# Performance work log

Measured on AMD Instinct MI355X. Metric: run time of the kernel, lower is better.

## Reference

```python
import jax, jax.numpy as jnp
import numpy as np


def setup_inputs() -> dict:
    key = jax.random.key(0)
    k1, k2, k3 = jax.random.split(key, 3)
    N, F, C, E = 100000, 256, 64, 3200000
    x = jax.random.normal(k1, (N, F), dtype=jnp.float32)
    edge_index = jax.random.randint(k2, (2, E), 0, N, dtype=jnp.int64)
    W = jax.random.normal(k3, (F, C), dtype=jnp.float32) * (1.0 / np.sqrt(F))
    b = jnp.zeros((C,), dtype=jnp.float32)
    return {"x": x, "edge_index": edge_index, "W": W, "b": b}


def reference(x, edge_index, W, b):
    N = x.shape[0]
    # Linear transform first (GCNConv: x @ W)
    xw = x @ W  # [N, C]
    # gcn_norm: add self-loops with weight 1
    loops = jnp.arange(N, dtype=edge_index.dtype)
    src = jnp.concatenate([edge_index[0], loops])
    dst = jnp.concatenate([edge_index[1], loops])
    ones = jnp.ones(src.shape[0], dtype=xw.dtype)
    deg = jax.ops.segment_sum(ones, dst, num_segments=N)  # in-degree incl. self-loop
    deg_inv_sqrt = jnp.where(deg > 0, jax.lax.rsqrt(deg), 0.0)
    norm = deg_inv_sqrt[src] * deg_inv_sqrt[dst]  # [E+N]
    # Message: norm * x_j, then MEAN aggregation over destinations (aggr='mean')
    msg = xw[src] * norm[:, None]  # [E+N, C]
    agg = jax.ops.segment_sum(msg, dst, num_segments=N)  # [N, C]
    cnt = jnp.maximum(deg, 1.0)  # number of incoming messages per node
    out = agg / cnt[:, None] + b
    return jax.nn.log_softmax(out, axis=1)
```

## Files before the change

kernel.cpp:

```cpp
#include <hip/hip_runtime.h>


#define C_DIM 64
#define F_DIM 256
#define TILE 128
#define BIN_PT 16
#define BIN_TILE_E 4096
#define SORT_CAP 6144
#define SMEM_BYTES 36880

#if __has_builtin(__builtin_amdgcn_cvt_pk_f32_fp8) && __has_builtin(__builtin_amdgcn_cvt_pk_fp8_f32)
#define USE_FP8 1
#endif

typedef __attribute__((ext_vector_type(8))) short bf16x8;
typedef __attribute__((ext_vector_type(2))) short bf16x2;
typedef __attribute__((ext_vector_type(4))) float f32x4;
typedef __attribute__((ext_vector_type(2))) float f32x2;

static __device__ __forceinline__ unsigned short f2bf(float f) {
    unsigned int u = __float_as_uint(f);
    unsigned int r = (u + 0x7FFFu + ((u >> 16) & 1u)) >> 16;
    return (unsigned short)r;
}
static __device__ __forceinline__ float u2lo(unsigned int u) {
    return __uint_as_float(u << 16);
}
static __device__ __forceinline__ float u2hi(unsigned int u) {
    return __uint_as_float(u & 0xFFFF0000u);
}

#if !defined(USE_FP8)
#if __has_builtin(__builtin_amdgcn_fdot2_f32_bf16)
static __device__ __forceinline__ void acc_pair(unsigned int u, float& lo, float& hi) {
    union { unsigned int ui; bf16x2 v; } p;
    p.ui = u;
    const bf16x2 SEL_LO = { (short)0x3F80, (short)0 };
    const bf16x2 SEL_HI = { (short)0, (short)0x3F80 };
    lo = __builtin_amdgcn_fdot2_f32_bf16(p.v, SEL_LO, lo, false);
    hi = __builtin_amdgcn_fdot2_f32_bf16(p.v, SEL_HI, hi, false);
}
#else
static __device__ __forceinline__ void acc_pair(unsigned int u, float& lo, float& hi) {
    lo += u2lo(u);
    hi += u2hi(u);
}
#endif
#endif


__global__ void k_zero1(int* __restrict__ a, int N) {
    int i = blockIdx.x * blockDim.x + threadIdx.x;
    if (i < N) a[i] = 0;
}

__global__ void k_zero2(int* __restrict__ a, int* __restrict__ b, int N) {
    int i = blockIdx.x * blockDim.x + threadIdx.x;
    if (i < N) { a[i] = 0; b[i] = 0; }
}

__global__ void k_count(const int* __restrict__ ei, int* __restrict__ degE, int E) {
    int stride = gridDim.x * blockDim.x;
    for (int e = blockIdx.x * blockDim.x + threadIdx.x; e < E; e += stride)
        atomicAdd(&degE[ei[E + e]], 1);
}

__global__ void k_dis2(const int* __restrict__ degE, float* __restrict__ dis, int N) {
    int i = blockIdx.x * blockDim.x + threadIdx.x;
    if (i < N) dis[i] = rsqrtf((float)(degE[i] + 1));
}


__global__ void k_prep(const float* __restrict__ W, unsigned short* __restrict__ Wt,
                       int* __restrict__ gcur, int K) {
    int i = blockIdx.x * blockDim.x + threadIdx.x;
    int c = i & 63, k = i >> 6;
    Wt[(size_t)c * F_DIM + k] = f2bf(W[(size_t)k * C_DIM + c]);
    if (i < K) gcur[i] = i * SORT_CAP;
}


__launch_bounds__(256)
__global__ void k_bin_gemm(const int* __restrict__ ei, int* __restrict__ gcur,
                           unsigned int* __restrict__ colb,
                           const float* __restrict__ x,
                           const unsigned short* __restrict__ Wt,
                           void* __restrict__ yout,
                           int E, int K, int nTiles, int gemmBlocks, int N) {
    __shared__ __align__(16) char smem[SMEM_BYTES];
    const int t = threadIdx.x;

    if (blockIdx.x < gemmBlocks) {
        float4 (*xs2)[1024] = (float4 (*)[1024])smem;
        const int wv   = t >> 6;
        const int lane = t & 63;
        const int lr   = lane & 15;
        const int lq   = lane >> 4;
        const int row0 = blockIdx.x * 64;

        auto stagefn = [&](int buf, int kk) {
            #pragma unroll
            for (int j = 0; j < 4; ++j) {
                int base_idx = j * 256 + wv * 64;
                int idx = base_idx + lane;
                int r   = idx >> 4;
                int c4  = idx & 15;
                int sc4 = c4 ^ (r & 15);
                int gr  = row0 + r;
                if (gr >= N) gr = N - 1;
                const float* g = x + (size_t)gr * F_DIM + kk * 64 + sc4 * 4;
                float4* lbase = &xs2[buf][base_idx];
                __builtin_amdgcn_global_load_lds(
                    (const __attribute__((address_space(1))) unsigned int*)g,
                    (__attribute__((address_space(3))) unsigned int*)lbase,
                    16, 0, 0);
            }
        };

        f32x4 acc[4] = {};

        stagefn(0, 0);
        __syncthreads();

        for (int kk = 0; kk < 4; ++kk) {
            if (kk < 3) stagefn((kk + 1) & 1, kk + 1);

            const float4* rowp = &xs2[kk & 1][(wv * 16 + lr) * 16];
            #pragma unroll
            for (int kc2 = 0; kc2 < 2; ++kc2) {
                int c4 = kc2 * 8 + lq * 2;
                float4 f0 = rowp[c4 ^ lr];
                float4 f1 = rowp[(c4 + 1) ^ lr];
                union { bf16x8 v; unsigned int u[4]; } a;
                a.u[0] = (unsigned)f2bf(f0.x) | ((unsigned)f2bf(f0.y) << 16);
                a.u[1] = (unsigned)f2bf(f0.z) | ((unsigned)f2bf(f0.w) << 16);
                a.u[2] = (unsigned)f2bf(f1.x) | ((unsigned)f2bf(f1.y) << 16);
                a.u[3] = (unsigned)f2bf(f1.z) | ((unsigned)f2bf(f1.w) << 16);
                const int kglob = kk * 64 + kc2 * 32 + lq * 8;
                #pragma unroll
                for (int cb = 0; cb < 4; ++cb) {
                    bf16x8 bfr = *(const bf16x8*)(Wt + (size_t)(cb * 16 + lr) * F_DIM + kglob);
                    acc[cb] = __builtin_amdgcn_mfma_f32_16x16x32_bf16(a.v, bfr, acc[cb], 0, 0, 0);
                }
            }
            __syncthreads();
        }

        const int rbase = row0 + wv * 16 + lq * 4;
        #pragma unroll
        for (int j = 0; j < 4; ++j) {
            int r = rbase + j;
            if (r < N) {
#ifdef USE_FP8
                unsigned char* yf = (unsigned char*)yout;
                #pragma unroll
                for (int cb = 0; cb < 4; ++cb) {
                    float v = acc[cb][j];
                    int p = __builtin_amdgcn_cvt_pk_fp8_f32(v, v, 0, false);
                    yf[(size_t)r * C_DIM + cb * 16 + lr] = (unsigned char)(p & 0xFF);
                }
#else
                unsigned short* ybp = (unsigned short*)yout;
                #pragma unroll
                for (int cb = 0; cb < 4; ++cb)
                    ybp[(size_t)r * C_DIM + cb * 16 + lr] = f2bf(acc[cb][j]);
#endif
            }
        }
        return;
    }

    {
        int* hcnt  = (int*)smem;
        int* hoff  = (int*)(smem + 4096);
        int* gbase = (int*)(smem + 8192);
        int* wps   = (int*)(smem + 12288);
        unsigned int*  stage    = (unsigned int*)(smem + 12304);
        unsigned short* stage_bk = (unsigned short*)(smem + 28688);
        const int wv = t >> 6;
        const int ln = t & 63;

        const int e0 = (blockIdx.x - gemmBlocks) * BIN_TILE_E;
        const int nE = min(BIN_TILE_E, E - e0);
        hcnt[t] = 0; hcnt[t + 256] = 0; hcnt[t + 512] = 0; hcnt[t + 768] = 0;
        __syncthreads();

        unsigned int pk[BIN_PT];
        int bk[BIN_PT];
        int off[BIN_PT];
        #pragma unroll
        for (int j = 0; j < BIN_PT; ++j) {
            int e = e0 + j * 256 + t;
            if (e < E) {
                int s = ei[e];
                int d = ei[E + e];
                int k = d >> 7;
                bk[j]  = k;
                pk[j]  = ((unsigned)(d & 127) << 25) | (unsigned)s;
                off[j] = atomicAdd(&hcnt[k], 1);
            } else bk[j] = -1;
        }
        __syncthreads();

        int a0 = hcnt[t*4], a1 = hcnt[t*4+1], a2 = hcnt[t*4+2], a3 = hcnt[t*4+3];
        int s4 = a0 + a1 + a2 + a3;
        int incl = s4;
        #pragma unroll
        for (int o = 1; o < 64; o <<= 1) {
            int u = __shfl_up(incl, o, 64);
            if (ln >= o) incl += u;
        }
        if (ln == 63) wps[wv] = incl;
        __syncthreads();
        int wpre = 0;
        #pragma unroll
        for (int w = 0; w < 4; ++w)
            if (w < wv) wpre += wps[w];
        int eb = wpre + incl - s4;
        hoff[t*4+0] = eb;
        hoff[t*4+1] = eb + a0;
        hoff[t*4+2] = eb + a0 + a1;
        hoff[t*4+3] = eb + a0 + a1 + a2;
        __syncthreads();

        #pragma unroll
        for (int j = 0; j < BIN_PT; ++j)
            if (bk[j] >= 0) {
                int p = hoff[bk[j]] + off[j];
                stage[p] = pk[j];
                stage_bk[p] = (unsigned short)bk[j];
            }

        for (int kq = t; kq < K; kq += 256) {
            int c = hcnt[kq];
            gbase[kq] = (c > 0) ? atomicAdd(&gcur[kq], c) : 0;
        }
        __syncthreads();

        for (int i = t; i < nE; i += 256) {
            int bb = stage_bk[i];
            int idx = gbase[bb] + (i - hoff[bb]);
            if (idx < (bb + 1) * SORT_CAP)
                colb[idx] = stage[i];
        }
    }
}


__launch_bounds__(256)
__global__ void k_sort(unsigned int* __restrict__ colb,
                       const int* __restrict__ gcur,
                       int* __restrict__ rowptr, int* __restrict__ rowcnt,
                       float* __restrict__ dis,
                       unsigned int* __restrict__ yw,
                       int N, int K) {
    __shared__ unsigned int scache[SORT_CAP];
    __shared__ int ncnt[TILE];
    __shared__ int nscan[TILE];
    __shared__ int ncur[TILE];
    __shared__ float sdis[TILE];
    const int t = threadIdx.x;
    const int k = blockIdx.x;
    const int base = k * SORT_CAP;
    const int cnt  = min(gcur[k] - base, SORT_CAP);
    const int node0 = k << 7;

    if (t < TILE) ncnt[t] = 0;
    __syncthreads();
    for (int i = t; i < cnt; i += 256) {
        unsigned int pk = colb[base + i];
        scache[i] = pk;
        atomicAdd(&ncnt[pk >> 25], 1);
    }
    __syncthreads();

    if (t < TILE) nscan[t] = ncnt[t];
    __syncthreads();
    for (int o = 1; o < TILE; o <<= 1) {
        int v = 0;
        if (t < TILE && t >= o) v = nscan[t - o];
        __syncthreads();
        if (t < TILE) nscan[t] += v;
        __syncthreads();
    }
    if (t < TILE) {
        int ex = nscan[t] - ncnt[t];
        ncur[t] = ex;
        int node = node0 + t;
        if (node < N) {
            rowptr[node] = base + ex;
            rowcnt[node] = ncnt[t];
            float d = rsqrtf((float)(ncnt[t] + 1));
            dis[node] = d;
            sdis[t] = d;
        }
    }
    __syncthreads();

    for (int i = t; i < cnt; i += 256) {
        unsigned int pk = scache[i];
        int dl  = (int)(pk >> 25);
        int pos = atomicAdd(&ncur[dl], 1);
        colb[base + pos] = pk & 0x1FFFFFFu;
    }

    const int nrows = min(TILE, N - node0);
#ifdef USE_FP8
    unsigned int* yrow = yw + (size_t)node0 * 16;
    for (int u = t; u < nrows * 16; u += 256) {
        int r = u >> 4;
        float d = sdis[r];
        unsigned int v = yrow[u];
        f32x2 lo = __builtin_amdgcn_cvt_pk_f32_fp8((int)v, false);
        f32x2 hi = __builtin_amdgcn_cvt_pk_f32_fp8((int)v, true);
        int p = __builtin_amdgcn_cvt_pk_fp8_f32(lo.x * d, lo.y * d, 0, false);
        p = __builtin_amdgcn_cvt_pk_fp8_f32(hi.x * d, hi.y * d, p, true);
        yrow[u] = (unsigned int)p;
    }
#else
    unsigned int* yrow = yw + (size_t)node0 * 32;
    for (int u = t; u < nrows * 32; u += 256) {
        int r = u >> 5;
        unsigned int v = yrow[u];
        float d = sdis[r];
        unsigned short lo = f2bf(u2lo(v) * d);
        unsigned short hi = f2bf(u2hi(v) * d);
        yrow[u] = ((unsigned int)hi << 16) | lo;
    }
#endif
}


__launch_bounds__(256)
__global__ void k_agg(const int* __restrict__ rowptr, const int* __restrict__ rowcnt,
                      const int* __restrict__ col,
                      const void* __restrict__ yin, const float* __restrict__ dis,
                      const float* __restrict__ b, float* __restrict__ out, int N) {
    const int lane = threadIdx.x & 63;
    const int g    = lane >> 3;
    const int cl   = lane & 7;
    int row = blockIdx.x * 4 + (threadIdx.x >> 6);
    if (row >= N) return;
    const int start = rowptr[row];
    const int cntE  = rowcnt[row];
    const int end   = start + cntE;

    float a0, a1, a2, a3, a4, a5, a6, a7;

#ifdef USE_FP8
    const uint2* yv = (const uint2*)yin;
    f32x2 p01 = {0.f, 0.f}, p23 = {0.f, 0.f}, p45 = {0.f, 0.f}, p67 = {0.f, 0.f};
    if (g == 0) {
        uint2 u = yv[(size_t)row * 8 + cl];
        p01 = __builtin_amdgcn_cvt_pk_f32_fp8((int)u.x, false);
        p23 = __builtin_amdgcn_cvt_pk_f32_fp8((int)u.x, true);
        p45 = __builtin_amdgcn_cvt_pk_f32_fp8((int)u.y, false);
        p67 = __builtin_amdgcn_cvt_pk_f32_fp8((int)u.y, true);
    }
    int i = start + g;
    for (; i + 24 < end; i += 32) {
        int s[4];
        #pragma unroll
        for (int j = 0; j < 4; ++j) s[j] = col[i + 8 * j];
        uint2 v[4];
        #pragma unroll
        for (int j = 0; j < 4; ++j) v[j] = yv[(size_t)s[j] * 8 + cl];
        #pragma unroll
        for (int j = 0; j < 4; ++j) {
            p01 += __builtin_amdgcn_cvt_pk_f32_fp8((int)v[j].x, false);
            p23 += __builtin_amdgcn_cvt_pk_f32_fp8((int)v[j].x, true);
            p45 += __builtin_amdgcn_cvt_pk_f32_fp8((int)v[j].y, false);
            p67 += __builtin_amdgcn_cvt_pk_f32_fp8((int)v[j].y, true);
        }
    }
    for (; i < end; i += 8) {
        uint2 u = yv[(size_t)col[i] * 8 + cl];
        p01 += __builtin_amdgcn_cvt_pk_f32_fp8((int)u.x, false);
        p23 += __builtin_amdgcn_cvt_pk_f32_fp8((int)u.x, true);
        p45 += __builtin_amdgcn_cvt_pk_f32_fp8((int)u.y, false);
        p67 += __builtin_amdgcn_cvt_pk_f32_fp8((int)u.y, true);
    }
    a0 = p01.x; a1 = p01.y; a2 = p23.x; a3 = p23.y;
    a4 = p45.x; a5 = p45.y; a6 = p67.x; a7 = p67.y;
#else
    const uint4* yv = (const uint4*)yin;
    a0 = a1 = a2 = a3 = a4 = a5 = a6 = a7 = 0.f;
    if (g == 0) {
        uint4 u = yv[(size_t)row * 8 + cl];
        a0 = u2lo(u.x); a1 = u2hi(u.x); a2 = u2lo(u.y); a3 = u2hi(u.y);
        a4 = u2lo(u.z); a5 = u2hi(u.z); a6 = u2lo(u.w); a7 = u2hi(u.w);
    }
    int i = start + g;
    for (; i + 24 < end; i += 32) {
        int s[4];
        #pragma unroll
        for (int j = 0; j < 4; ++j) s[j] = col[i + 8 * j];
        uint4 v[4];
        #pragma unroll
        for (int j = 0; j < 4; ++j) v[j] = yv[(size_t)s[j] * 8 + cl];
        #pragma unroll
        for (int j = 0; j < 4; ++j) {
            acc_pair(v[j].x, a0, a1);
            acc_pair(v[j].y, a2, a3);
            acc_pair(v[j].z, a4, a5);
            acc_pair(v[j].w, a6, a7);
        }
    }
    for (; i < end; i += 8) {
        uint4 u = yv[(size_t)col[i] * 8 + cl];
        acc_pair(u.x, a0, a1);
        acc_pair(u.y, a2, a3);
        acc_pair(u.z, a4, a5);
        acc_pair(u.w, a6, a7);
    }
#endif

    #pragma unroll
    for (int o = 8; o <= 32; o <<= 1) {
        a0 += __shfl_xor(a0, o, 64); a1 += __shfl_xor(a1, o, 64);
        a2 += __shfl_xor(a2, o, 64); a3 += __shfl_xor(a3, o, 64);
        a4 += __shfl_xor(a4, o, 64); a5 += __shfl_xor(a5, o, 64);
        a6 += __shfl_xor(a6, o, 64); a7 += __shfl_xor(a7, o, 64);
    }

    const float scale = dis[row] / (float)(cntE + 1);
    const float4 b0 = *(const float4*)&b[8 * cl];
    const float4 b1 = *(const float4*)&b[8 * cl + 4];
    float v0 = a0 * scale + b0.x;
    float v1 = a1 * scale + b0.y;
    float v2 = a2 * scale + b0.z;
    float v3 = a3 * scale + b0.w;
    float v4 = a4 * scale + b1.x;
    float v5 = a5 * scale + b1.y;
    float v6 = a6 * scale + b1.z;
    float v7 = a7 * scale + b1.w;

    float m = fmaxf(fmaxf(fmaxf(v0, v1), fmaxf(v2, v3)),
                    fmaxf(fmaxf(v4, v5), fmaxf(v6, v7)));
    #pragma unroll
    for (int o = 4; o >= 1; o >>= 1) m = fmaxf(m, __shfl_xor(m, o, 64));
    float ss = __expf(v0 - m) + __expf(v1 - m) + __expf(v2 - m) + __expf(v3 - m)
             + __expf(v4 - m) + __expf(v5 - m) + __expf(v6 - m) + __expf(v7 - m);
    #pragma unroll
    for (int o = 4; o >= 1; o >>= 1) ss += __shfl_xor(ss, o, 64);
    float lg = logf(ss);

    if (g == 0) {
        float* orow = out + (size_t)row * C_DIM + 8 * cl;
        *(float4*)(orow + 0) = make_float4(v0 - m - lg, v1 - m - lg, v2 - m - lg, v3 - m - lg);
        *(float4*)(orow + 4) = make_float4(v4 - m - lg, v5 - m - lg, v6 - m - lg, v7 - m - lg);
    }
}


__launch_bounds__(256, 4)
__global__ void k_gemmF(const float* __restrict__ x, const float* __restrict__ W,
                        const float* __restrict__ dis, float* __restrict__ y, int N) {
    __shared__ float xs[64 * 68];
    __shared__ float ws[64 * 64];
    const int t   = threadIdx.x;
    const int c16 = t & 15;
    const int rg  = t >> 4;
    const int row0 = blockIdx.x * 64;

    float acc[4][4] = {};

    for (int kk = 0; kk < F_DIM / 64; ++kk) {
        {
            int r  = t >> 2;
            int fq = (t & 3) * 16;
            int grow = row0 + r;
            float4 v0, v1, v2, v3;
            if (grow < N) {
                const float* src = x + (long long)grow * F_DIM + kk * 64 + fq;
                v0 = *(const float4*)(src + 0);
                v1 = *(const float4*)(src + 4);
                v2 = *(const float4*)(src + 8);
                v3 = *(const float4*)(src + 12);
            } else {
                v0 = v1 = v2 = v3 = make_float4(0.f, 0.f, 0.f, 0.f);
            }
            float4* dstp = (float4*)&xs[r * 68 + fq];
            dstp[0] = v0; dstp[1] = v1; dstp[2] = v2; dstp[3] = v3;
        }
        {
            int f  = t >> 2;
            int cq = (t & 3) * 16;
            const float* src = W + (long long)(kk * 64 + f) * C_DIM + cq;
            float4* dstp = (float4*)&ws[f * 64 + cq];
            dstp[0] = *(const float4*)(src + 0);
            dstp[1] = *(const float4*)(src + 4);
            dstp[2] = *(const float4*)(src + 8);
            dstp[3] = *(const float4*)(src + 12);
        }
        __syncthreads();

        const float4* xs4 = (const float4*)xs;
        const float4* ws4 = (const float4*)ws;
        #pragma unroll
        for (int f4 = 0; f4 < 16; ++f4) {
            float xr[4][4];
            #pragma unroll
            for (int k = 0; k < 4; ++k) {
                float4 v = xs4[(rg * 4 + k) * 17 + f4];
                xr[k][0] = v.x; xr[k][1] = v.y; xr[k][2] = v.z; xr[k][3] = v.w;
            }
            #pragma unroll
            for (int j = 0; j < 4; ++j) {
                float4 wv = ws4[(f4 * 4 + j) * 16 + c16];
                #pragma unroll
                for (int k = 0; k < 4; ++k) {
                    acc[k][0] += xr[k][j] * wv.x;
                    acc[k][1] += xr[k][j] * wv.y;
                    acc[k][2] += xr[k][j] * wv.z;
                    acc[k][3] += xr[k][j] * wv.w;
                }
            }
        }
        __syncthreads();
    }

    const int c = c16 * 4;
    #pragma unroll
    for (int k = 0; k < 4; ++k) {
        int row = row0 + rg * 4 + k;
        if (row < N) {
            float dd = dis[row];
            float4 v = make_float4(acc[k][0]*dd, acc[k][1]*dd, acc[k][2]*dd, acc[k][3]*dd);
            *(float4*)&y[(size_t)row * C_DIM + c] = v;
        }
    }
}

__global__ void k_scan_blk(const int* __restrict__ degE, int* __restrict__ excl,
                           int* __restrict__ bsum, int N) {
    __shared__ int sm[1024];
    const int tid = threadIdx.x;
    int i = blockIdx.x * 1024 + tid;
    int v = (i < N) ? degE[i] : 0;
    sm[tid] = v;
    __syncthreads();
    for (int off = 1; off < 1024; off <<= 1) {
        int t = (tid >= off) ? sm[tid - off] : 0;
        __syncthreads();
        sm[tid] += t;
        __syncthreads();
    }
    int incl = sm[tid];
    if (i < N) excl[i] = incl - v;
    if (tid == 1023) bsum[blockIdx.x] = incl;
}

__global__ void k_scan_top(int* __restrict__ bs, int nblk) {
    __shared__ int sm[128];
    const int tid = threadIdx.x;
    int v = (tid < nblk) ? bs[tid] : 0;
    sm[tid] = v;
    __syncthreads();
    for (int off = 1; off < 128; off <<= 1) {
        int t = (tid >= off) ? sm[tid - off] : 0;
        __syncthreads();
        sm[tid] += t;
        __syncthreads();
    }
    if (tid < nblk) bs[tid] = sm[tid] - v;
}

__global__ void k_scan_add(const int* __restrict__ excl, const int* __restrict__ bs,
                           int* __restrict__ rowptr, int N, int E) {
    int i = blockIdx.x * blockDim.x + threadIdx.x;
    if (i < N) rowptr[i] = excl[i] + bs[i >> 10];
    if (i == 0) rowptr[N] = E;
}

__global__ void k_scatter(const int* __restrict__ ei, const int* __restrict__ rowptr,
                          int* __restrict__ cnt, int* __restrict__ col, int E) {
    int stride = gridDim.x * blockDim.x;
    for (int e = blockIdx.x * blockDim.x + threadIdx.x; e < E; e += stride) {
        int s = ei[e];
        int d = ei[E + e];
        int p = atomicAdd(&cnt[d], 1);
        col[rowptr[d] + p] = s;
    }
}

__global__ void k_aggB(const int* __restrict__ rowptr, const int* __restrict__ col,
                       const float* __restrict__ y, const float* __restrict__ dis,
                       const float* __restrict__ b, float* __restrict__ out, int N) {
    const int lane = threadIdx.x & 63;
    int row = blockIdx.x * 4 + (threadIdx.x >> 6);
    if (row >= N) return;
    const int start = rowptr[row], end = rowptr[row + 1];
    float acc = y[(size_t)row * C_DIM + lane];
    for (int i = start; i < end; ++i) acc += y[(size_t)col[i] * C_DIM + lane];
    float val = acc * dis[row] / (float)(end - start + 1) + b[lane];
    float m = val;
    #pragma unroll
    for (int o = 32; o >= 1; o >>= 1) m = fmaxf(m, __shfl_xor(m, o, 64));
    float ex = expf(val - m);
    float ss = ex;
    #pragma unroll
    for (int o = 32; o >= 1; o >>= 1) ss += __shfl_xor(ss, o, 64);
    out[(size_t)row * C_DIM + lane] = val - m - logf(ss);
}

__global__ void k_selfloop2(const float* __restrict__ y, const float* __restrict__ dis,
                            float* __restrict__ agg, int NC) {
    int i = blockIdx.x * blockDim.x + threadIdx.x;
    if (i < NC) agg[i] = dis[i >> 6] * y[i];
}

__launch_bounds__(256)
__global__ void k_edge2(const int* __restrict__ ei, const float* __restrict__ y,
                        const float* __restrict__ dis, float* __restrict__ agg, int E) {
    const int lane = threadIdx.x & 63;
    int wid = (blockIdx.x * blockDim.x + threadIdx.x) >> 6;
    int nw  = (gridDim.x * blockDim.x) >> 6;
    for (int e = wid; e < E; e += nw) {
        int s = ei[e];
        int d = ei[E + e];
        atomicAdd(&agg[(size_t)d * C_DIM + lane], y[(size_t)s * C_DIM + lane] * dis[d]);
    }
}

__launch_bounds__(256)
__global__ void k_final2(float* __restrict__ agg, const int* __restrict__ degE,
                         const float* __restrict__ b, int N) {
    const int lane = threadIdx.x & 63;
    int row = blockIdx.x * 4 + (threadIdx.x >> 6);
    if (row >= N) return;
    float v = agg[(size_t)row * C_DIM + lane] / (float)(degE[row] + 1) + b[lane];
    float m = v;
    #pragma unroll
    for (int o = 32; o >= 1; o >>= 1) m = fmaxf(m, __shfl_xor(m, o, 64));
    float ex = expf(v - m);
    float ss = ex;
    #pragma unroll
    for (int o = 32; o >= 1; o >>= 1) ss += __shfl_xor(ss, o, 64);
    agg[(size_t)row * C_DIM + lane] = v - m - logf(ss);
}


extern "C" void kernel_launch(void* const* d_in, const int* in_sizes, int n_in,
                              void* d_out, int out_size, void* d_ws, size_t ws_size,
                              hipStream_t stream) {
    const float* x  = (const float*)d_in[0];
    const int*   ei = (const int*)d_in[1];
    const float* W  = (const float*)d_in[2];
    const float* b  = (const float*)d_in[3];

    const int C = in_sizes[3];
    const int F = in_sizes[2] / C;
    const int N = in_sizes[0] / F;
    const int E = in_sizes[1] / 2;

    float* out = (float*)d_out;
    char*  wsb = (char*)d_ws;

    const int K    = (N + TILE - 1) / TILE;
    const int nblk = (N + 1023) / 1024;

    size_t offA = 0;
    void*  yv   = (void*)(wsb + offA);    offA += ((size_t)N * C * 2 + 15) & ~15ull;
    unsigned short* Wt = (unsigned short*)(wsb + offA); offA += ((size_t)F * C * 2 + 15) & ~15ull;
    float* disA   = (float*)(wsb + offA); offA += (size_t)N * 4;
    int*   rowptrA= (int*)(wsb + offA);   offA += (size_t)N * 4;
    int*   rowcntA= (int*)(wsb + offA);   offA += (size_t)N * 4;
    int*   gcur   = (int*)(wsb + offA);   offA += (size_t)K * 4;
    unsigned int* colb = (unsigned int*)(wsb + offA); offA += (size_t)K * SORT_CAP * 4;

    size_t offB = 0;
    float* yB     = (float*)(wsb + offB); offB += (size_t)N * C * 4;
    float* disB   = (float*)(wsb + offB); offB += (size_t)N * 4;
    int*   rowptrB= (int*)(wsb + offB);   offB += ((size_t)N + 1) * 4;
    int*   degE   = (int*)(wsb + offB);   offB += (size_t)N * 4;
    int*   cntB   = (int*)(wsb + offB);   offB += (size_t)N * 4;
    int*   excl   = (int*)(wsb + offB);   offB += (size_t)nblk * 1024 * 4;
    int*   bsum   = (int*)(wsb + offB);   offB += 128 * 4;
    int*   colB   = (int*)(wsb + offB);   offB += (size_t)E * 4;

    const bool okA = (offA <= ws_size) && (K <= 1024) && (N < (1 << 25)) &&
                     (C == 64) && (F == 256) &&
                     ((long long)E < (long long)K * SORT_CAP);
    const bool okB = (offB <= ws_size) && (nblk <= 128);

    const dim3 B256(256);
    const dim3 gN((N + 255) / 256);
    const int nTiles = (E + BIN_TILE_E - 1) / BIN_TILE_E;
    const int gemmBlocks = (N + 63) / 64;

    if (okA) {
        hipLaunchKernelGGL(k_prep,     dim3((F * C + 255) / 256), B256, 0, stream,
                           W, Wt, gcur, K);
        hipLaunchKernelGGL(k_bin_gemm, dim3(gemmBlocks + nTiles), B256, 0, stream,
                           ei, gcur, colb, x, Wt, yv, E, K, nTiles, gemmBlocks, N);
        hipLaunchKernelGGL(k_sort,     dim3(K), B256, 0, stream, colb, gcur,
                           rowptrA, rowcntA, disA, (unsigned int*)yv, N, K);
        hipLaunchKernelGGL(k_agg,      dim3((N + 3) / 4), B256, 0, stream,
                           rowptrA, rowcntA, (const int*)colb,
                           (const void*)yv, disA, b, out, N);
    } else if (okB) {
        hipLaunchKernelGGL(k_zero2,    gN, B256, 0, stream, degE, cntB, N);
        hipLaunchKernelGGL(k_count,    dim3(2048), B256, 0, stream, ei, degE, E);
        hipLaunchKernelGGL(k_dis2,     gN, B256, 0, stream, degE, disB, N);
        hipLaunchKernelGGL(k_scan_blk, dim3(nblk), dim3(1024), 0, stream, degE, excl, bsum, N);
        hipLaunchKernelGGL(k_scan_top, dim3(1), dim3(128), 0, stream, bsum, nblk);
        hipLaunchKernelGGL(k_scan_add, gN, B256, 0, stream, excl, bsum, rowptrB, N, E);
        hipLaunchKernelGGL(k_gemmF,    dim3(gemmBlocks), B256, 0, stream, x, W, disB, yB, N);
        hipLaunchKernelGGL(k_scatter,  dim3(2048), B256, 0, stream, ei, rowptrB, cntB, colB, E);
        hipLaunchKernelGGL(k_aggB,     dim3((N + 3) / 4), B256, 0, stream,
                           rowptrB, colB, yB, disB, b, out, N);
    } else {
        hipLaunchKernelGGL(k_zero1,     gN, B256, 0, stream, degE, N);
        hipLaunchKernelGGL(k_count,     dim3(2048), B256, 0, stream, ei, degE, E);
        hipLaunchKernelGGL(k_dis2,      gN, B256, 0, stream, degE, disB, N);
        hipLaunchKernelGGL(k_gemmF,     dim3(gemmBlocks), B256, 0, stream, x, W, disB, yB, N);
        hipLaunchKernelGGL(k_selfloop2, dim3(((size_t)N * C + 255) / 256), B256, 0, stream,
                           yB, disB, out, N * C);
        hipLaunchKernelGGL(k_edge2,     dim3(4096), B256, 0, stream, ei, yB, disB, out, E);
        hipLaunchKernelGGL(k_final2,    dim3((N + 3) / 4), B256, 0, stream, out, degE, b, N);
    }
}
```

Measured before the change: 148.3 us.

## Split fused bin+GEMM kernel and fold degree scaling into GEMM epilogue

Breaks the combined binning/GEMM kernel into a standalone binning kernel and a separate MFMA GEMM that runs after the sort. Because the degree normalisation is already known when the GEMM runs, the GEMM scales each row by dis before quantising. This removes the read-modify-write pass over y in k_sort and the double rounding it caused. In exchange, binning and GEMM no longer overlap within one launch, and there is one more kernel launch on the stream.

Result: slower. 161.4 us (+8.8%).

```diff
diff --git a/kernel.cpp b/kernel.cpp
--- a/kernel.cpp
+++ b/kernel.cpp
@@ -7,7 +7,6 @@
 #define BIN_PT 16
 #define BIN_TILE_E 4096
 #define SORT_CAP 6144
-#define SMEM_BYTES 36880
 
 #if __has_builtin(__builtin_amdgcn_cvt_pk_f32_fp8) && __has_builtin(__builtin_amdgcn_cvt_pk_fp8_f32)
 #define USE_FP8 1
@@ -81,106 +80,20 @@
 
 
 __launch_bounds__(256)
-__global__ void k_bin_gemm(const int* __restrict__ ei, int* __restrict__ gcur,
-                           unsigned int* __restrict__ colb,
-                           const float* __restrict__ x,
-                           const unsigned short* __restrict__ Wt,
-                           void* __restrict__ yout,
-                           int E, int K, int nTiles, int gemmBlocks, int N) {
-    __shared__ __align__(16) char smem[SMEM_BYTES];
+__global__ void k_bin(const int* __restrict__ ei, int* __restrict__ gcur,
+                      unsigned int* __restrict__ colb, int E, int K, int nTiles) {
+    __shared__ int hcnt[1024];
+    __shared__ int hoff[1024];
+    __shared__ int gbase[1024];
+    __shared__ int wps[4];
+    __shared__ unsigned int stage[BIN_TILE_E];
+    __shared__ unsigned short stage_bk[BIN_TILE_E];
     const int t = threadIdx.x;
-
-    if (blockIdx.x < gemmBlocks) {
-        float4 (*xs2)[1024] = (float4 (*)[1024])smem;
-        const int wv   = t >> 6;
-        const int lane = t & 63;
-        const int lr   = lane & 15;
-        const int lq   = lane >> 4;
-        const int row0 = blockIdx.x * 64;
-
-        auto stagefn = [&](int buf, int kk) {
-            #pragma unroll
-            for (int j = 0; j < 4; ++j) {
-                int base_idx = j * 256 + wv * 64;
-                int idx = base_idx + lane;
-                int r   = idx >> 4;
-                int c4  = idx & 15;
-                int sc4 = c4 ^ (r & 15);
-                int gr  = row0 + r;
-                if (gr >= N) gr = N - 1;
-                const float* g = x + (size_t)gr * F_DIM + kk * 64 + sc4 * 4;
-                float4* lbase = &xs2[buf][base_idx];
-                __builtin_amdgcn_global_load_lds(
-                    (const __attribute__((address_space(1))) unsigned int*)g,
-                    (__attribute__((address_space(3))) unsigned int*)lbase,
-                    16, 0, 0);
-            }
-        };
-
-        f32x4 acc[4] = {};
-
-        stagefn(0, 0);
-        __syncthreads();
-
-        for (int kk = 0; kk < 4; ++kk) {
-            if (kk < 3) stagefn((kk + 1) & 1, kk + 1);
-
-            const float4* rowp = &xs2[kk & 1][(wv * 16 + lr) * 16];
-            #pragma unroll
-            for (int kc2 = 0; kc2 < 2; ++kc2) {
-                int c4 = kc2 * 8 + lq * 2;
-                float4 f0 = rowp[c4 ^ lr];
-                float4 f1 = rowp[(c4 + 1) ^ lr];
-                union { bf16x8 v; unsigned int u[4]; } a;
-                a.u[0] = (unsigned)f2bf(f0.x) | ((unsigned)f2bf(f0.y) << 16);
-                a.u[1] = (unsigned)f2bf(f0.z) | ((unsigned)f2bf(f0.w) << 16);
-                a.u[2] = (unsigned)f2bf(f1.x) | ((unsigned)f2bf(f1.y) << 16);
-                a.u[3] = (unsigned)f2bf(f1.z) | ((unsigned)f2bf(f1.w) << 16);
-                const int kglob = kk * 64 + kc2 * 32 + lq * 8;
-                #pragma unroll
-                for (int cb = 0; cb < 4; ++cb) {
-                    bf16x8 bfr = *(const bf16x8*)(Wt + (size_t)(cb * 16 + lr) * F_DIM + kglob);
-                    acc[cb] = __builtin_amdgcn_mfma_f32_16x16x32_bf16(a.v, bfr, acc[cb], 0, 0, 0);
-                }
-            }
-            __syncthreads();
-        }
-
-        const int rbase = row0 + wv * 16 + lq * 4;
-        #pragma unroll
-        for (int j = 0; j < 4; ++j) {
-            int r = rbase + j;
-            if (r < N) {
-#ifdef USE_FP8
-                unsigned char* yf = (unsigned char*)yout;
-                #pragma unroll
-                for (int cb = 0; cb < 4; ++cb) {
-                    float v = acc[cb][j];
-                    int p = __builtin_amdgcn_cvt_pk_fp8_f32(v, v, 0, false);
-                    yf[(size_t)r * C_DIM + cb * 16 + lr] = (unsigned char)(p & 0xFF);
-                }
-#else
-                unsigned short* ybp = (unsigned short*)yout;
-                #pragma unroll
-                for (int cb = 0; cb < 4; ++cb)
-                    ybp[(size_t)r * C_DIM + cb * 16 + lr] = f2bf(acc[cb][j]);
-#endif
-            }
-        }
-        return;
-    }
-
-    {
-        int* hcnt  = (int*)smem;
-        int* hoff  = (int*)(smem + 4096);
-        int* gbase = (int*)(smem + 8192);
-        int* wps   = (int*)(smem + 12288);
-        unsigned int*  stage    = (unsigned int*)(smem + 12304);
-        unsigned short* stage_bk = (unsigned short*)(smem + 28688);
-        const int wv = t >> 6;
-        const int ln = t & 63;
-
-        const int e0 = (blockIdx.x - gemmBlocks) * BIN_TILE_E;
+    const int wv = t >> 6;
+    const int ln = t & 63;
+
+    for (int tile = blockIdx.x; tile < nTiles; tile += gridDim.x) {
+        const int e0 = tile * BIN_TILE_E;
         const int nE = min(BIN_TILE_E, E - e0);
         hcnt[t] = 0; hcnt[t + 256] = 0; hcnt[t + 512] = 0; hcnt[t + 768] = 0;
         __syncthreads();
@@ -243,6 +156,7 @@
             if (idx < (bb + 1) * SORT_CAP)
                 colb[idx] = stage[i];
         }
+        __syncthreads();
     }
 }
 
@@ -251,14 +165,11 @@
 __global__ void k_sort(unsigned int* __restrict__ colb,
                        const int* __restrict__ gcur,
                        int* __restrict__ rowptr, int* __restrict__ rowcnt,
-                       float* __restrict__ dis,
-                       unsigned int* __restrict__ yw,
-                       int N, int K) {
+                       float* __restrict__ dis, int N, int K) {
     __shared__ unsigned int scache[SORT_CAP];
     __shared__ int ncnt[TILE];
     __shared__ int nscan[TILE];
     __shared__ int ncur[TILE];
-    __shared__ float sdis[TILE];
     const int t = threadIdx.x;
     const int k = blockIdx.x;
     const int base = k * SORT_CAP;
@@ -290,9 +201,7 @@
         if (node < N) {
             rowptr[node] = base + ex;
             rowcnt[node] = ncnt[t];
-            float d = rsqrtf((float)(ncnt[t] + 1));
-            dis[node] = d;
-            sdis[t] = d;
+            dis[node] = rsqrtf((float)(ncnt[t] + 1));
         }
     }
     __syncthreads();
@@ -303,31 +212,92 @@
         int pos = atomicAdd(&ncur[dl], 1);
         colb[base + pos] = pk & 0x1FFFFFFu;
     }
-
-    const int nrows = min(TILE, N - node0);
+}
+
+
+__launch_bounds__(256)
+__global__ void k_gemm_mfma(const float* __restrict__ x,
+                            const unsigned short* __restrict__ Wt,
+                            const float* __restrict__ dis,
+                            void* __restrict__ yout, int N) {
+    __shared__ float4 xs2[2][1024];
+    const int t    = threadIdx.x;
+    const int wv   = t >> 6;
+    const int lane = t & 63;
+    const int lr   = lane & 15;
+    const int lq   = lane >> 4;
+    const int row0 = blockIdx.x * 64;
+
+    auto stagefn = [&](int buf, int kk) {
+        #pragma unroll
+        for (int j = 0; j < 4; ++j) {
+            int base_idx = j * 256 + wv * 64;
+            int idx = base_idx + lane;
+            int r   = idx >> 4;
+            int c4  = idx & 15;
+            int sc4 = c4 ^ (r & 15);
+            int gr  = row0 + r;
+            if (gr >= N) gr = N - 1;
+            const float* g = x + (size_t)gr * F_DIM + kk * 64 + sc4 * 4;
+            float4* lbase = &xs2[buf][base_idx];
+            __builtin_amdgcn_global_load_lds(
+                (const __attribute__((address_space(1))) unsigned int*)g,
+                (__attribute__((address_space(3))) unsigned int*)lbase,
+                16, 0, 0);
+        }
+    };
+
+    f32x4 acc[4] = {};
+
+    stagefn(0, 0);
+    __syncthreads();
+
+    for (int kk = 0; kk < 4; ++kk) {
+        if (kk < 3) stagefn((kk + 1) & 1, kk + 1);
+
+        const float4* rowp = &xs2[kk & 1][(wv * 16 + lr) * 16];
+        #pragma unroll
+        for (int kc2 = 0; kc2 < 2; ++kc2) {
+            int c4 = kc2 * 8 + lq * 2;
+            float4 f0 = rowp[c4 ^ lr];
+            float4 f1 = rowp[(c4 + 1) ^ lr];
+            union { bf16x8 v; unsigned int u[4]; } a;
+            a.u[0] = (unsigned)f2bf(f0.x) | ((unsigned)f2bf(f0.y) << 16);
+            a.u[1] = (unsigned)f2bf(f0.z) | ((unsigned)f2bf(f0.w) << 16);
+            a.u[2] = (unsigned)f2bf(f1.x) | ((unsigned)f2bf(f1.y) << 16);
+            a.u[3] = (unsigned)f2bf(f1.z) | ((unsigned)f2bf(f1.w) << 16);
+            const int kglob = kk * 64 + kc2 * 32 + lq * 8;
+            #pragma unroll
+            for (int cb = 0; cb < 4; ++cb) {
+                bf16x8 bfr = *(const bf16x8*)(Wt + (size_t)(cb * 16 + lr) * F_DIM + kglob);
+                acc[cb] = __builtin_amdgcn_mfma_f32_16x16x32_bf16(a.v, bfr, acc[cb], 0, 0, 0);
+            }
+        }
+        __syncthreads();
+    }
+
+    const int rbase = row0 + wv * 16 + lq * 4;
+    #pragma unroll
+    for (int j = 0; j < 4; ++j) {
+        int r = rbase + j;
+        if (r < N) {
+            float dd = dis[r];
 #ifdef USE_FP8
-    unsigned int* yrow = yw + (size_t)node0 * 16;
-    for (int u = t; u < nrows * 16; u += 256) {
-        int r = u >> 4;
-        float d = sdis[r];
-        unsigned int v = yrow[u];
-        f32x2 lo = __builtin_amdgcn_cvt_pk_f32_fp8((int)v, false);
-        f32x2 hi = __builtin_amdgcn_cvt_pk_f32_fp8((int)v, true);
-        int p = __builtin_amdgcn_cvt_pk_fp8_f32(lo.x * d, lo.y * d, 0, false);
-        p = __builtin_amdgcn_cvt_pk_fp8_f32(hi.x * d, hi.y * d, p, true);
-        yrow[u] = (unsigned int)p;
-    }
+            unsigned char* yf = (unsigned char*)yout;
+            #pragma unroll
+            for (int cb = 0; cb < 4; ++cb) {
+                float v = acc[cb][j] * dd;
+                int p = __builtin_amdgcn_cvt_pk_fp8_f32(v, v, 0, false);
+                yf[(size_t)r * C_DIM + cb * 16 + lr] = (unsigned char)(p & 0xFF);
+            }
 #else
-    unsigned int* yrow = yw + (size_t)node0 * 32;
-    for (int u = t; u < nrows * 32; u += 256) {
-        int r = u >> 5;
-        unsigned int v = yrow[u];
-        float d = sdis[r];
-        unsigned short lo = f2bf(u2lo(v) * d);
-        unsigned short hi = f2bf(u2hi(v) * d);
-        yrow[u] = ((unsigned int)hi << 16) | lo;
-    }
+            unsigned short* ybp = (unsigned short*)yout;
+            #pragma unroll
+            for (int cb = 0; cb < 4; ++cb)
+                ybp[(size_t)r * C_DIM + cb * 16 + lr] = f2bf(acc[cb][j] * dd);
 #endif
+        }
+    }
 }
 
 
@@ -690,13 +660,15 @@
     const int gemmBlocks = (N + 63) / 64;
 
     if (okA) {
-        hipLaunchKernelGGL(k_prep,     dim3((F * C + 255) / 256), B256, 0, stream,
+        hipLaunchKernelGGL(k_prep,      dim3((F * C + 255) / 256), B256, 0, stream,
                            W, Wt, gcur, K);
-        hipLaunchKernelGGL(k_bin_gemm, dim3(gemmBlocks + nTiles), B256, 0, stream,
-                           ei, gcur, colb, x, Wt, yv, E, K, nTiles, gemmBlocks, N);
-        hipLaunchKernelGGL(k_sort,     dim3(K), B256, 0, stream, colb, gcur,
-                           rowptrA, rowcntA, disA, (unsigned int*)yv, N, K);
-        hipLaunchKernelGGL(k_agg,      dim3((N + 3) / 4), B256, 0, stream,
+        hipLaunchKernelGGL(k_bin,       dim3(nTiles), B256, 0, stream, ei, gcur, colb,
+                           E, K, nTiles);
+        hipLaunchKernelGGL(k_sort,      dim3(K), B256, 0, stream, colb, gcur,
+                           rowptrA, rowcntA, disA, N, K);
+        hipLaunchKernelGGL(k_gemm_mfma, dim3(gemmBlocks), B256, 0, stream,
+                           x, Wt, disA, yv, N);
+        hipLaunchKernelGGL(k_agg,       dim3((N + 3) / 4), B256, 0, stream,
                            rowptrA, rowcntA, (const int*)colb,
                            (const void*)yv, disA, b, out, N);
     } else if (okB) {
```
